# Kernel tuning notes

Hardware: AMD Instinct MI355X
Metric: run time of the kernel (lower is better)

The kernel has to match this reference:

```python
import jax, jax.numpy as jnp
import numpy as np

MAX_WARPING_WINDOW = None  # matches init kwarg (None => full window, no masking)


def _pairwise_euclidean(x, y):
    # x: (B, F, Tx), y: (B, F, Ty) -> (B, Tx, Ty)
    # ||x_t - y_s||_2 computed via the expanded quadratic form (one GEMM instead
    # of materializing the (B, F, Tx, Ty) difference tensor like the torch code).
    x2 = jnp.sum(x * x, axis=1)                      # (B, Tx)
    y2 = jnp.sum(y * y, axis=1)                      # (B, Ty)
    xy = jnp.einsum('bft,bfs->bts', x, y)            # (B, Tx, Ty)
    d2 = jnp.maximum(x2[:, :, None] + y2[:, None, :] - 2.0 * xy, 0.0)
    return jnp.sqrt(d2)


def _dtw(cost):
    # cost: (B, Tx, Ty). Classic DTW DP:
    #   dtw[i, j] = cost[i-1, j-1] + min(dtw[i-1, j], dtw[i, j-1], dtw[i-1, j-1])
    # outer scan over rows i, inner scan over columns j (carries dtw[i, j-1]).
    B, Tx, Ty = cost.shape
    dt = cost.dtype
    INF = jnp.array(jnp.inf, dt)
    cost_t = jnp.transpose(cost, (1, 2, 0))          # (Tx, Ty, B)

    def row_step(carry, cost_row):
        prev_row, left = carry                       # prev_row: (Ty, B) = dtw[i-1, 1:], left: (B,) = dtw[i-1, 0]
        prev_shift = jnp.concatenate([left[None, :], prev_row[:-1]], axis=0)  # dtw[i-1, j-1]
        a = jnp.minimum(prev_row, prev_shift)        # min(dtw[i-1, j], dtw[i-1, j-1])

        def col_step(cur_left, ac):
            a_j, c_j = ac                            # each (B,)
            cur = c_j + jnp.minimum(a_j, cur_left)   # cur_left = dtw[i, j-1]
            return cur, cur

        _, cur_row = jax.lax.scan(col_step, jnp.full((B,), INF, dt), (a, cost_row))
        return (cur_row, jnp.full((B,), INF, dt)), None

    # row 0 of the DP: dtw[0, 0] = 0, dtw[0, j>0] = inf
    init = (jnp.full((Ty, B), INF, dt), jnp.zeros((B,), dt))
    (last_row, _), _ = jax.lax.scan(row_step, init, cost_t)
    return last_row[-1]                              # dtw[Tx, Ty], shape (B,)


def setup_inputs() -> dict:
    key = jax.random.key(0)
    kx, ky = jax.random.split(key)
    B, F, T = 128, 128, 512
    x = jax.random.normal(kx, (B, F, T), dtype=jnp.float32)
    y = jax.random.normal(ky, (B, F, T), dtype=jnp.float32)
    return {"x": x, "y": y}


def reference(x, y):
    cost = _pairwise_euclidean(x, y)                 # (B, Tx, Ty)
    if MAX_WARPING_WINDOW is not None:
        Tx, Ty = cost.shape[1], cost.shape[2]
        p = jnp.arange(Tx)[:, None]
        q = jnp.arange(Ty)[None, :]
        cost = jnp.where(jnp.abs(p - q) <= MAX_WARPING_WINDOW, cost, jnp.inf)
    return _dtw(cost)
```

## Files before the change

kernel.cpp:

```cpp
#include <hip/hip_runtime.h>
#include <stdint.h>

#define B_ 128
#define F_ 128
#define T_ 512
#define TS 64
#define DIAG_N 1024

#define BIGV 1e30f

typedef __attribute__((ext_vector_type(8))) short     bf16x8;
typedef __attribute__((ext_vector_type(4))) float     f32x4;

static __device__ __forceinline__ unsigned short f32_to_bf16(float f) {
    union { float f; uint32_t u; } v; v.f = f;
    const uint32_t u = v.u + 0x7fffu + ((v.u >> 16) & 1u);
    return (unsigned short)(u >> 16);
}

static __device__ __forceinline__ float wave_shr1(float src, float fill) {
    const int r = __builtin_amdgcn_update_dpp(
        __builtin_bit_cast(int, fill), __builtin_bit_cast(int, src),
        0x138 , 0xf, 0xf, false);
    return __builtin_bit_cast(float, r);
}
static __device__ __forceinline__ float wave_shl1(float src, float fill) {
    const int r = __builtin_amdgcn_update_dpp(
        __builtin_bit_cast(int, fill), __builtin_bit_cast(int, src),
        0x130 , 0xf, 0xf, false);
    return __builtin_bit_cast(float, r);
}

#define FMIX_LO(dst, h, m)                                                  \
    asm("v_fma_mix_f32 %0, %1, 1.0, %2 op_sel:[0,0,0] op_sel_hi:[1,0,0]"    \
        : "=v"(dst) : "v"(h), "v"(m))
#define FMIX_HI(dst, h, m)                                                  \
    asm("v_fma_mix_f32 %0, %1, 1.0, %2 op_sel:[1,0,0] op_sel_hi:[1,0,0]"    \
        : "=v"(dst) : "v"(h), "v"(m))

__global__ __launch_bounds__(256) void dtw_prep_kernel(
    const float* __restrict__ x, const float* __restrict__ y,
    unsigned short* __restrict__ xt, unsigned short* __restrict__ yt,
    float* __restrict__ nx, float* __restrict__ ny)
{
    const int tch = blockIdx.x;
    const int b   = blockIdx.y;
    const int z   = blockIdx.z;
    const int tid = threadIdx.x;
    const int t0  = tch * 64;

    const float* src      = (z == 0 ? x : y) + (size_t)b * F_ * T_;
    unsigned short* dst   = (z == 0 ? xt : yt) + (size_t)b * T_ * F_;
    float* nd             = (z == 0 ? nx : ny) + (size_t)b * T_;

    __shared__ float S[F_][65];

    const int fr = tid >> 4;
    const int q  = (tid & 15) * 4;
#pragma unroll
    for (int p = 0; p < 8; ++p) {
        const int f = p * 16 + fr;
        const float4 v = *(const float4*)(src + (size_t)f * T_ + t0 + q);
        S[f][q] = v.x; S[f][q + 1] = v.y; S[f][q + 2] = v.z; S[f][q + 3] = v.w;
    }
    __syncthreads();

    if (tid < 64) {
        float s = 0.f;
#pragma unroll
        for (int f = 0; f < F_; ++f) { const float v = S[f][tid]; s = fmaf(v, v, s); }
        nd[t0 + tid] = s;
    }

    const int tl = tid >> 2;
    const int fb = (tid & 3) * 32;
    uint32_t pk[16];
#pragma unroll
    for (int e = 0; e < 16; ++e) {
        const uint32_t lo = f32_to_bf16(S[fb + 2 * e][tl]);
        const uint32_t hi = f32_to_bf16(S[fb + 2 * e + 1][tl]);
        pk[e] = lo | (hi << 16);
    }
    uint32_t* o = (uint32_t*)(dst + (size_t)(t0 + tl) * F_ + fb);
#pragma unroll
    for (int e = 0; e < 16; e += 4)
        *(uint4*)(o + e) = make_uint4(pk[e], pk[e + 1], pk[e + 2], pk[e + 3]);
}

__global__ __launch_bounds__(256) void dtw_cost_kernel(
    const unsigned short* __restrict__ xt, const unsigned short* __restrict__ yt,
    const float* __restrict__ nx, const float* __restrict__ ny,
    unsigned short* __restrict__ costD, int b0)
{
    const int tj  = blockIdx.x;
    const int ti  = blockIdx.y;
    const int bl  = blockIdx.z;
    const int b   = b0 + bl;
    const int tid = threadIdx.x;
    const int gi0 = ti * TS;
    const int gj0 = tj * TS;

    const int w    = tid >> 6;
    const int lane = tid & 63;
    const int l15  = lane & 15;
    const int hi   = lane >> 4;

    __shared__ __align__(16) char smem[16384];
    unsigned short* Ys = (unsigned short*)smem;

    {
        const int l16 = tid & 15;
#pragma unroll
        for (int p = 0; p < 4; ++p) {
            const int row = p * 16 + (tid >> 4);
            const uint4 vy = *(const uint4*)(yt + ((size_t)b * T_ + gj0 + row) * F_ + l16 * 8);
            const int byt = (row * 256 + l16 * 16) ^ ((row & 7) << 4);
            *(uint4*)((char*)Ys + byt) = vy;
        }
    }

    const unsigned short* xb = xt + ((size_t)b * T_ + gi0 + 16 * w + l15) * F_ + hi * 8;
    const bf16x8 A0 = *(const bf16x8*)(xb);
    const bf16x8 A1 = *(const bf16x8*)(xb + 32);
    const bf16x8 A2 = *(const bf16x8*)(xb + 64);
    const bf16x8 A3 = *(const bf16x8*)(xb + 96);

    const float4 x2r = *(const float4*)(nx + (size_t)b * T_ + gi0 + 16 * w + 4 * hi);
    float y2c[4];
#pragma unroll
    for (int nt = 0; nt < 4; ++nt)
        y2c[nt] = ny[(size_t)b * T_ + gj0 + nt * 16 + l15];
    const float x2v[4] = {x2r.x, x2r.y, x2r.z, x2r.w};

    __syncthreads();

    f32x4 acc[4] = {};
#pragma unroll
    for (int kb = 0; kb < 4; ++kb) {
        const int koff = kb * 64 + hi * 16;
        const bf16x8 a = (kb == 0) ? A0 : (kb == 1) ? A1 : (kb == 2) ? A2 : A3;
#pragma unroll
        for (int nt = 0; nt < 4; ++nt) {
            const int col = nt * 16 + l15;
            const bf16x8 bb = *(const bf16x8*)((const char*)Ys +
                               ((col * 256 + koff) ^ ((col & 7) << 4)));
            acc[nt] = __builtin_amdgcn_mfma_f32_16x16x32_bf16(a, bb, acc[nt], 0, 0, 0);
        }
    }

    __syncthreads();
    unsigned short* Ts = (unsigned short*)smem;
#pragma unroll
    for (int nt = 0; nt < 4; ++nt) {
        const int col = nt * 16 + l15;
#pragma unroll
        for (int r = 0; r < 4; ++r) {
            const int row = 16 * w + hi * 4 + r;
            const float c = sqrtf(fmaxf(x2v[r] + y2c[nt] - 2.f * acc[nt][r], 0.f));
            const _Float16 hv = (_Float16)c;
            Ts[row * 67 + col] = *(const unsigned short*)&hv;
        }
    }
    __syncthreads();

    unsigned short* outD = costD + (size_t)bl * (DIAG_N * (size_t)T_);
    const int tbase = gi0 + gj0;
#pragma unroll
    for (int q = 0; q < 16; ++q) {
        const int g = q * 4 + w;
        const int d = (lane <= g) ? g : g + 64;
        outD[(size_t)(tbase + d) * T_ + gj0 + lane] = Ts[(d - lane) * 67 + lane];
    }
}

__global__ __launch_bounds__(128, 1) void dtw_dp_bidi(
    const unsigned short* __restrict__ costD, float* __restrict__ out, int b0)
{
    const int bl  = blockIdx.x;
    const int tid = threadIdx.x;
    const int w   = tid >> 6;
    const int L   = tid & 63;
    const unsigned short* gbase = costD + (size_t)bl * (DIAG_N * (size_t)T_) + 8 * L;

    __shared__ __align__(16) unsigned short ringF[32][T_];
    __shared__ __align__(16) unsigned short ringB[32][T_];
    __shared__ __align__(16) float bb2[T_];
    __shared__ __align__(16) float bb3[T_];

    float va0 = BIGV, va1 = BIGV, va2 = BIGV, va3 = BIGV,
          va4 = BIGV, va5 = BIGV, va6 = BIGV, va7 = BIGV;
    float vb0 = BIGV, vb1 = BIGV, vb2 = BIGV, vb3 = BIGV,
          vb4 = BIGV, vb5 = BIGV, vb6 = BIGV, vb7 = BIGV;
    float s2c;
    uint4 ca0, ca1, ca2, ca3, ca4, ca5, ca6, ca7;
    uint4 cb0, cb1, cb2, cb3, cb4, cb5, cb6, cb7;

#define GLD(RING, row, slot)                                                \
    __builtin_amdgcn_global_load_lds(                                       \
        (const __attribute__((address_space(1))) void*)(gbase + (size_t)(row) * T_), \
        (__attribute__((address_space(3))) void*)(&RING[slot][0]), 16, 0, 0)

#define GLD8F(blk) do {                                                     \
    const int r0_ = (blk) * 8, s0_ = ((blk) & 3) * 8;                       \
    GLD(ringF, r0_ + 0, s0_ + 0); GLD(ringF, r0_ + 1, s0_ + 1);             \
    GLD(ringF, r0_ + 2, s0_ + 2); GLD(ringF, r0_ + 3, s0_ + 3);             \
    GLD(ringF, r0_ + 4, s0_ + 4); GLD(ringF, r0_ + 5, s0_ + 5);             \
    GLD(ringF, r0_ + 6, s0_ + 6); GLD(ringF, r0_ + 7, s0_ + 7);             \
} while (0)

#define GLD8B(blk) do {                                                     \
    const int v0_ = (blk) * 8, s0_ = ((blk) & 3) * 8;                       \
    GLD(ringB, 1022 - (v0_ + 0), s0_ + 0); GLD(ringB, 1022 - (v0_ + 1), s0_ + 1); \
    GLD(ringB, 1022 - (v0_ + 2), s0_ + 2); GLD(ringB, 1022 - (v0_ + 3), s0_ + 3); \
    GLD(ringB, 1022 - (v0_ + 4), s0_ + 4); GLD(ringB, 1022 - (v0_ + 5), s0_ + 5); \
    GLD(ringB, 1022 - (v0_ + 6), s0_ + 6); GLD(ringB, 1022 - (v0_ + 7), s0_ + 7); \
} while (0)

#define WAITV(n)                                                            \
    do { asm volatile("s_waitcnt vmcnt(" #n ")" ::: "memory");              \
         __builtin_amdgcn_sched_barrier(0); } while (0)

#define SB __builtin_amdgcn_sched_barrier(0)

#define RL8(RING, BK, blk) do {                                             \
    const unsigned short* rp_ = &RING[((blk) & 3) * 8][8 * L];              \
    BK##0 = *(const uint4*)(rp_ + 0 * T_);                                  \
    BK##1 = *(const uint4*)(rp_ + 1 * T_);                                  \
    BK##2 = *(const uint4*)(rp_ + 2 * T_);                                  \
    BK##3 = *(const uint4*)(rp_ + 3 * T_);                                  \
    BK##4 = *(const uint4*)(rp_ + 4 * T_);                                  \
    BK##5 = *(const uint4*)(rp_ + 5 * T_);                                  \
    BK##6 = *(const uint4*)(rp_ + 6 * T_);                                  \
    BK##7 = *(const uint4*)(rp_ + 7 * T_);                                  \
} while (0)

#define STEPF_A(Hv) do {                                                    \
    const float s1 = wave_shr1(va7, BIGV);                                  \
    float n0, n1, n2, n3, n4, n5, n6, n7;                                   \
    FMIX_LO(n0, Hv.x, fminf(fminf(va0, s1),  s2c));                         \
    FMIX_HI(n1, Hv.x, fminf(fminf(va1, va0), vb0));                         \
    FMIX_LO(n2, Hv.y, fminf(fminf(va2, va1), vb1));                         \
    FMIX_HI(n3, Hv.y, fminf(fminf(va3, va2), vb2));                         \
    FMIX_LO(n4, Hv.z, fminf(fminf(va4, va3), vb3));                         \
    FMIX_HI(n5, Hv.z, fminf(fminf(va5, va4), vb4));                         \
    FMIX_LO(n6, Hv.w, fminf(fminf(va6, va5), vb5));                         \
    FMIX_HI(n7, Hv.w, fminf(fminf(va7, va6), vb6));                         \
    s2c = s1;                                                               \
    vb0 = n0; vb1 = n1; vb2 = n2; vb3 = n3;                                 \
    vb4 = n4; vb5 = n5; vb6 = n6; vb7 = n7;                                 \
} while (0)

#define STEPF_B(Hv) do {                                                    \
    const float s1 = wave_shr1(vb7, BIGV);                                  \
    float n0, n1, n2, n3, n4, n5, n6, n7;                                   \
    FMIX_LO(n0, Hv.x, fminf(fminf(vb0, s1),  s2c));                         \
    FMIX_HI(n1, Hv.x, fminf(fminf(vb1, vb0), va0));                         \
    FMIX_LO(n2, Hv.y, fminf(fminf(vb2, vb1), va1));                         \
    FMIX_HI(n3, Hv.y, fminf(fminf(vb3, vb2), va2));                         \
    FMIX_LO(n4, Hv.z, fminf(fminf(vb4, vb3), va3));                         \
    FMIX_HI(n5, Hv.z, fminf(fminf(vb5, vb4), va4));                         \
    FMIX_LO(n6, Hv.w, fminf(fminf(vb6, vb5), va5));                         \
    FMIX_HI(n7, Hv.w, fminf(fminf(vb7, vb6), va6));                         \
    s2c = s1;                                                               \
    va0 = n0; va1 = n1; va2 = n2; va3 = n3;                                 \
    va4 = n4; va5 = n5; va6 = n6; va7 = n7;                                 \
} while (0)

#define STEPB_A(Hv) do {                                                    \
    const float s1 = wave_shl1(va0, BIGV);                                  \
    float n0, n1, n2, n3, n4, n5, n6, n7;                                   \
    FMIX_HI(n7, Hv.w, fminf(fminf(va7, s1),  s2c));                         \
    FMIX_LO(n6, Hv.w, fminf(fminf(va6, va7), vb7));                         \
    FMIX_HI(n5, Hv.z, fminf(fminf(va5, va6), vb6));                         \
    FMIX_LO(n4, Hv.z, fminf(fminf(va4, va5), vb5));                         \
    FMIX_HI(n3, Hv.y, fminf(fminf(va3, va4), vb4));                         \
    FMIX_LO(n2, Hv.y, fminf(fminf(va2, va3), vb3));                         \
    FMIX_HI(n1, Hv.x, fminf(fminf(va1, va2), vb2));                         \
    FMIX_LO(n0, Hv.x, fminf(fminf(va0, va1), vb1));                         \
    s2c = s1;                                                               \
    vb0 = n0; vb1 = n1; vb2 = n2; vb3 = n3;                                 \
    vb4 = n4; vb5 = n5; vb6 = n6; vb7 = n7;                                 \
} while (0)

#define STEPB_B(Hv) do {                                                    \
    const float s1 = wave_shl1(vb0, BIGV);                                  \
    float n0, n1, n2, n3, n4, n5, n6, n7;                                   \
    FMIX_HI(n7, Hv.w, fminf(fminf(vb7, s1),  s2c));                         \
    FMIX_LO(n6, Hv.w, fminf(fminf(vb6, vb7), va7));                         \
    FMIX_HI(n5, Hv.z, fminf(fminf(vb5, vb6), va6));                         \
    FMIX_LO(n4, Hv.z, fminf(fminf(vb4, vb5), va5));                         \
    FMIX_HI(n3, Hv.y, fminf(fminf(vb3, vb4), va4));                         \
    FMIX_LO(n2, Hv.y, fminf(fminf(vb2, vb3), va3));                         \
    FMIX_HI(n1, Hv.x, fminf(fminf(vb1, vb2), va2));                         \
    FMIX_LO(n0, Hv.x, fminf(fminf(vb0, vb1), va1));                         \
    s2c = s1;                                                               \
    va0 = n0; va1 = n1; va2 = n2; va3 = n3;                                 \
    va4 = n4; va5 = n5; va6 = n6; va7 = n7;                                 \
} while (0)

#define STEPF8(BK)                                                          \
    STEPF_A(BK##0); STEPF_B(BK##1); STEPF_A(BK##2); STEPF_B(BK##3);         \
    STEPF_A(BK##4); STEPF_B(BK##5); STEPF_A(BK##6); STEPF_B(BK##7)
#define STEPB8(BK)                                                          \
    STEPB_A(BK##0); STEPB_B(BK##1); STEPB_A(BK##2); STEPB_B(BK##3);         \
    STEPB_A(BK##4); STEPB_B(BK##5); STEPB_A(BK##6); STEPB_B(BK##7)

    if (w == 0) {
        s2c = (L == 0) ? 0.f : BIGV;
#pragma unroll
        for (int r = 0; r < 32; ++r) GLD(ringF, r, r);
        WAITV(24); RL8(ringF, ca, 0); SB;
        int k = 0;
#pragma unroll 1
        for (int it = 0; it < 30; ++it) {
            WAITV(16); RL8(ringF, cb, k + 1); SB; STEPF8(ca); SB; GLD8F(k + 4); SB;
            WAITV(16); RL8(ringF, ca, k + 2); SB; STEPF8(cb); SB; GLD8F(k + 5); SB;
            k += 2;
        }
        WAITV(16); RL8(ringF, cb, 61); SB; STEPF8(ca); SB;
        WAITV(8);  RL8(ringF, ca, 62); SB; STEPF8(cb); SB;
        WAITV(0);  RL8(ringF, cb, 63); SB; STEPF8(ca); SB;
        STEPF8(cb);
    } else {
        s2c = (L == 63) ? 0.f : BIGV;
#pragma unroll
        for (int r = 0; r < 32; ++r) GLD(ringB, 1022 - r, r);
        WAITV(24); RL8(ringB, ca, 0); SB;
        int k = 0;
#pragma unroll 1
        for (int it = 0; it < 30; ++it) {
            WAITV(16); RL8(ringB, cb, k + 1); SB; STEPB8(ca); SB; GLD8B(k + 4); SB;
            WAITV(16); RL8(ringB, ca, k + 2); SB; STEPB8(cb); SB; GLD8B(k + 5); SB;
            k += 2;
        }
        WAITV(16); RL8(ringB, cb, 61); SB; STEPB8(ca); SB;
        WAITV(8);  RL8(ringB, ca, 62); SB; STEPB8(cb); SB;
        WAITV(0);  RL8(ringB, cb, 63); SB; STEPB8(ca); SB;
        STEPB_A(cb0); STEPB_B(cb1); STEPB_A(cb2); STEPB_B(cb3);
        STEPB_A(cb4); STEPB_B(cb5); STEPB_A(cb6);
        *(float4*)&bb2[8 * L]     = make_float4(vb0, vb1, vb2, vb3);
        *(float4*)&bb2[8 * L + 4] = make_float4(vb4, vb5, vb6, vb7);
        *(float4*)&bb3[8 * L]     = make_float4(va0, va1, va2, va3);
        *(float4*)&bb3[8 * L + 4] = make_float4(va4, va5, va6, va7);
    }

    __syncthreads();

    if (w == 0) {
        const float4 p0 = *(const float4*)&bb2[8 * L];
        const float4 p1 = *(const float4*)&bb2[8 * L + 4];
        const float4 q0 = *(const float4*)&bb3[8 * L];
        const float4 q1 = *(const float4*)&bb3[8 * L + 4];
        const float b2[8] = {p0.x, p0.y, p0.z, p0.w, p1.x, p1.y, p1.z, p1.w};
        const float b3[8] = {q0.x, q0.y, q0.z, q0.w, q1.x, q1.y, q1.z, q1.w};
        const float F511[8] = {va0, va1, va2, va3, va4, va5, va6, va7};
        const float F510[8] = {vb0, vb1, vb2, vb3, vb4, vb5, vb6, vb7};
        float b2s[8], b3s[8];
#pragma unroll
        for (int kk = 0; kk < 7; ++kk) { b2s[kk] = b2[kk + 1]; b3s[kk] = b3[kk + 1]; }
        b2s[7] = wave_shl1(b2[0], BIGV);
        b3s[7] = wave_shl1(b3[0], BIGV);
        float m = BIGV;
#pragma unroll
        for (int kk = 0; kk < 8; ++kk) {
            const float t1 = F511[kk] + fminf(fminf(b2[kk], b2s[kk]), b3s[kk]);
            const float t2 = F510[kk] + b2s[kk];
            m = fminf(m, fminf(t1, t2));
        }
#pragma unroll
        for (int off = 1; off < 64; off <<= 1)
            m = fminf(m, __shfl_xor(m, off));
        if (L == 0) out[b0 + bl] = m;
    }

#undef GLD
#undef GLD8F
#undef GLD8B
#undef WAITV
#undef SB
#undef RL8
#undef STEPF_A
#undef STEPF_B
#undef STEPB_A
#undef STEPB_B
#undef STEPF8
#undef STEPB8
}

extern "C" void kernel_launch(void* const* d_in, const int* in_sizes, int n_in,
                              void* d_out, int out_size, void* d_ws, size_t ws_size,
                              hipStream_t stream)
{
    const float* x = (const float*)d_in[0];
    const float* y = (const float*)d_in[1];
    float* out = (float*)d_out;

    unsigned short* xt = (unsigned short*)d_ws;
    unsigned short* yt = xt + (size_t)B_ * T_ * F_;
    float* nx = (float*)(yt + (size_t)B_ * T_ * F_);
    float* ny = nx + (size_t)B_ * T_;
    unsigned short* costD = (unsigned short*)(ny + (size_t)B_ * T_);
    const size_t head = (size_t)((char*)costD - (char*)d_ws);

    const size_t perb = (size_t)DIAG_N * T_ * sizeof(unsigned short);
    int Bg = 8;
    for (int g = 128; g >= 8; g >>= 1)
        if (ws_size >= head + perb * (size_t)g) { Bg = g; break; }

    hipLaunchKernelGGL(dtw_prep_kernel, dim3(T_ / 64, B_, 2), dim3(256), 0, stream,
                       x, y, xt, yt, nx, ny);

    for (int b0 = 0; b0 < B_; b0 += Bg) {
        dim3 gc(T_ / TS, T_ / TS, Bg);
        hipLaunchKernelGGL(dtw_cost_kernel, gc, dim3(256), 0, stream,
                           xt, yt, nx, ny, costD, b0);
        hipLaunchKernelGGL(dtw_dp_bidi, dim3(Bg), dim3(128), 0, stream,
                           costD, out, b0);
    }
}
```

Baseline: 99.10 us.

## Split bidirectional DTW DP into separate per-direction workgroups with global combine

The forward and backward DP waves, previously two waves in one 128-thread block, now run as separate 64-thread blocks (2*Bg blocks) so they can be placed on different CUs. The half-results go to a global scratch buffer and a new small combine kernel finishes the reduction. Each block gets a deeper 64-row LDS ring with eight blocks of loads in flight to hide global latency better. The cost is an extra kernel launch per batch group, a global round-trip for the boundary rows, and a slightly larger workspace per batch, which may reduce the chosen Bg.

New measurement: 105.9 us. 1.07x slower.

```diff
diff --git a/kernel.cpp b/kernel.cpp
--- a/kernel.cpp
+++ b/kernel.cpp
@@ -21,13 +21,13 @@
 static __device__ __forceinline__ float wave_shr1(float src, float fill) {
     const int r = __builtin_amdgcn_update_dpp(
         __builtin_bit_cast(int, fill), __builtin_bit_cast(int, src),
-        0x138 , 0xf, 0xf, false);
+        0x138, 0xf, 0xf, false);
     return __builtin_bit_cast(float, r);
 }
 static __device__ __forceinline__ float wave_shl1(float src, float fill) {
     const int r = __builtin_amdgcn_update_dpp(
         __builtin_bit_cast(int, fill), __builtin_bit_cast(int, src),
-        0x130 , 0xf, 0xf, false);
+        0x130, 0xf, 0xf, false);
     return __builtin_bit_cast(float, r);
 }
 
@@ -173,19 +173,15 @@
     }
 }
 
-__global__ __launch_bounds__(128, 1) void dtw_dp_bidi(
-    const unsigned short* __restrict__ costD, float* __restrict__ out, int b0)
+__global__ __launch_bounds__(64, 1) void dtw_dp_dir(
+    const unsigned short* __restrict__ costD, float* __restrict__ hand, int Bg)
 {
-    const int bl  = blockIdx.x;
-    const int tid = threadIdx.x;
-    const int w   = tid >> 6;
-    const int L   = tid & 63;
+    const int isB = (int)blockIdx.x >= Bg;
+    const int bl  = isB ? (int)blockIdx.x - Bg : (int)blockIdx.x;
+    const int L   = threadIdx.x;
     const unsigned short* gbase = costD + (size_t)bl * (DIAG_N * (size_t)T_) + 8 * L;
 
-    __shared__ __align__(16) unsigned short ringF[32][T_];
-    __shared__ __align__(16) unsigned short ringB[32][T_];
-    __shared__ __align__(16) float bb2[T_];
-    __shared__ __align__(16) float bb3[T_];
+    __shared__ __align__(16) unsigned short ring[64][T_];
 
     float va0 = BIGV, va1 = BIGV, va2 = BIGV, va3 = BIGV,
           va4 = BIGV, va5 = BIGV, va6 = BIGV, va7 = BIGV;
@@ -195,25 +191,25 @@
     uint4 ca0, ca1, ca2, ca3, ca4, ca5, ca6, ca7;
     uint4 cb0, cb1, cb2, cb3, cb4, cb5, cb6, cb7;
 
-#define GLD(RING, row, slot)                                                \
+#define GLD(row, slotrow)                                                   \
     __builtin_amdgcn_global_load_lds(                                       \
         (const __attribute__((address_space(1))) void*)(gbase + (size_t)(row) * T_), \
-        (__attribute__((address_space(3))) void*)(&RING[slot][0]), 16, 0, 0)
+        (__attribute__((address_space(3))) void*)(&ring[slotrow][0]), 16, 0, 0)
 
 #define GLD8F(blk) do {                                                     \
-    const int r0_ = (blk) * 8, s0_ = ((blk) & 3) * 8;                       \
-    GLD(ringF, r0_ + 0, s0_ + 0); GLD(ringF, r0_ + 1, s0_ + 1);             \
-    GLD(ringF, r0_ + 2, s0_ + 2); GLD(ringF, r0_ + 3, s0_ + 3);             \
-    GLD(ringF, r0_ + 4, s0_ + 4); GLD(ringF, r0_ + 5, s0_ + 5);             \
-    GLD(ringF, r0_ + 6, s0_ + 6); GLD(ringF, r0_ + 7, s0_ + 7);             \
+    const int r0_ = (blk) * 8, s0_ = ((blk) & 7) * 8;                       \
+    GLD(r0_ + 0, s0_ + 0); GLD(r0_ + 1, s0_ + 1);                           \
+    GLD(r0_ + 2, s0_ + 2); GLD(r0_ + 3, s0_ + 3);                           \
+    GLD(r0_ + 4, s0_ + 4); GLD(r0_ + 5, s0_ + 5);                           \
+    GLD(r0_ + 6, s0_ + 6); GLD(r0_ + 7, s0_ + 7);                           \
 } while (0)
 
 #define GLD8B(blk) do {                                                     \
-    const int v0_ = (blk) * 8, s0_ = ((blk) & 3) * 8;                       \
-    GLD(ringB, 1022 - (v0_ + 0), s0_ + 0); GLD(ringB, 1022 - (v0_ + 1), s0_ + 1); \
-    GLD(ringB, 1022 - (v0_ + 2), s0_ + 2); GLD(ringB, 1022 - (v0_ + 3), s0_ + 3); \
-    GLD(ringB, 1022 - (v0_ + 4), s0_ + 4); GLD(ringB, 1022 - (v0_ + 5), s0_ + 5); \
-    GLD(ringB, 1022 - (v0_ + 6), s0_ + 6); GLD(ringB, 1022 - (v0_ + 7), s0_ + 7); \
+    const int v0_ = (blk) * 8, s0_ = ((blk) & 7) * 8;                       \
+    GLD(1022 - (v0_ + 0), s0_ + 0); GLD(1022 - (v0_ + 1), s0_ + 1);         \
+    GLD(1022 - (v0_ + 2), s0_ + 2); GLD(1022 - (v0_ + 3), s0_ + 3);         \
+    GLD(1022 - (v0_ + 4), s0_ + 4); GLD(1022 - (v0_ + 5), s0_ + 5);         \
+    GLD(1022 - (v0_ + 6), s0_ + 6); GLD(1022 - (v0_ + 7), s0_ + 7);         \
 } while (0)
 
 #define WAITV(n)                                                            \
@@ -222,8 +218,8 @@
 
 #define SB __builtin_amdgcn_sched_barrier(0)
 
-#define RL8(RING, BK, blk) do {                                             \
-    const unsigned short* rp_ = &RING[((blk) & 3) * 8][8 * L];              \
+#define RL8(BK, blk) do {                                                   \
+    const unsigned short* rp_ = &ring[((blk) & 7) * 8][8 * L];              \
     BK##0 = *(const uint4*)(rp_ + 0 * T_);                                  \
     BK##1 = *(const uint4*)(rp_ + 1 * T_);                                  \
     BK##2 = *(const uint4*)(rp_ + 2 * T_);                                  \
@@ -305,72 +301,59 @@
     STEPB_A(BK##0); STEPB_B(BK##1); STEPB_A(BK##2); STEPB_B(BK##3);         \
     STEPB_A(BK##4); STEPB_B(BK##5); STEPB_A(BK##6); STEPB_B(BK##7)
 
-    if (w == 0) {
+    float* hb = hand + (size_t)bl * 4 * T_;
+
+    if (!isB) {
         s2c = (L == 0) ? 0.f : BIGV;
-#pragma unroll
-        for (int r = 0; r < 32; ++r) GLD(ringF, r, r);
-        WAITV(24); RL8(ringF, ca, 0); SB;
+        GLD8F(0); GLD8F(1); GLD8F(2); GLD8F(3);
+        GLD8F(4); GLD8F(5); GLD8F(6);
+        WAITV(48); RL8(ca, 0); SB;
+        GLD8F(7); SB;
         int k = 0;
 #pragma unroll 1
-        for (int it = 0; it < 30; ++it) {
-            WAITV(16); RL8(ringF, cb, k + 1); SB; STEPF8(ca); SB; GLD8F(k + 4); SB;
-            WAITV(16); RL8(ringF, ca, k + 2); SB; STEPF8(cb); SB; GLD8F(k + 5); SB;
+        for (int it = 0; it < 28; ++it) {
+            WAITV(48); RL8(cb, k + 1); SB; STEPF8(ca); SB; GLD8F(k + 8); SB;
+            WAITV(48); RL8(ca, k + 2); SB; STEPF8(cb); SB; GLD8F(k + 9); SB;
             k += 2;
         }
-        WAITV(16); RL8(ringF, cb, 61); SB; STEPF8(ca); SB;
-        WAITV(8);  RL8(ringF, ca, 62); SB; STEPF8(cb); SB;
-        WAITV(0);  RL8(ringF, cb, 63); SB; STEPF8(ca); SB;
+        WAITV(48); RL8(cb, 57); SB; STEPF8(ca); SB;
+        WAITV(40); RL8(ca, 58); SB; STEPF8(cb); SB;
+        WAITV(32); RL8(cb, 59); SB; STEPF8(ca); SB;
+        WAITV(24); RL8(ca, 60); SB; STEPF8(cb); SB;
+        WAITV(16); RL8(cb, 61); SB; STEPF8(ca); SB;
+        WAITV(8);  RL8(ca, 62); SB; STEPF8(cb); SB;
+        WAITV(0);  RL8(cb, 63); SB; STEPF8(ca); SB;
         STEPF8(cb);
+        *(float4*)(hb + 0 * T_ + 8 * L)     = make_float4(va0, va1, va2, va3);
+        *(float4*)(hb + 0 * T_ + 8 * L + 4) = make_float4(va4, va5, va6, va7);
+        *(float4*)(hb + 1 * T_ + 8 * L)     = make_float4(vb0, vb1, vb2, vb3);
+        *(float4*)(hb + 1 * T_ + 8 * L + 4) = make_float4(vb4, vb5, vb6, vb7);
     } else {
         s2c = (L == 63) ? 0.f : BIGV;
-#pragma unroll
-        for (int r = 0; r < 32; ++r) GLD(ringB, 1022 - r, r);
-        WAITV(24); RL8(ringB, ca, 0); SB;
+        GLD8B(0); GLD8B(1); GLD8B(2); GLD8B(3);
+        GLD8B(4); GLD8B(5); GLD8B(6);
+        WAITV(48); RL8(ca, 0); SB;
+        GLD8B(7); SB;
         int k = 0;
 #pragma unroll 1
-        for (int it = 0; it < 30; ++it) {
-            WAITV(16); RL8(ringB, cb, k + 1); SB; STEPB8(ca); SB; GLD8B(k + 4); SB;
-            WAITV(16); RL8(ringB, ca, k + 2); SB; STEPB8(cb); SB; GLD8B(k + 5); SB;
+        for (int it = 0; it < 28; ++it) {
+            WAITV(48); RL8(cb, k + 1); SB; STEPB8(ca); SB; GLD8B(k + 8); SB;
+            WAITV(48); RL8(ca, k + 2); SB; STEPB8(cb); SB; GLD8B(k + 9); SB;
             k += 2;
         }
-        WAITV(16); RL8(ringB, cb, 61); SB; STEPB8(ca); SB;
-        WAITV(8);  RL8(ringB, ca, 62); SB; STEPB8(cb); SB;
-        WAITV(0);  RL8(ringB, cb, 63); SB; STEPB8(ca); SB;
+        WAITV(48); RL8(cb, 57); SB; STEPB8(ca); SB;
+        WAITV(40); RL8(ca, 58); SB; STEPB8(cb); SB;
+        WAITV(32); RL8(cb, 59); SB; STEPB8(ca); SB;
+        WAITV(24); RL8(ca, 60); SB; STEPB8(cb); SB;
+        WAITV(16); RL8(cb, 61); SB; STEPB8(ca); SB;
+        WAITV(8);  RL8(ca, 62); SB; STEPB8(cb); SB;
+        WAITV(0);  RL8(cb, 63); SB; STEPB8(ca); SB;
         STEPB_A(cb0); STEPB_B(cb1); STEPB_A(cb2); STEPB_B(cb3);
         STEPB_A(cb4); STEPB_B(cb5); STEPB_A(cb6);
-        *(float4*)&bb2[8 * L]     = make_float4(vb0, vb1, vb2, vb3);
-        *(float4*)&bb2[8 * L + 4] = make_float4(vb4, vb5, vb6, vb7);
-        *(float4*)&bb3[8 * L]     = make_float4(va0, va1, va2, va3);
-        *(float4*)&bb3[8 * L + 4] = make_float4(va4, va5, va6, va7);
-    }
-
-    __syncthreads();
-
-    if (w == 0) {
-        const float4 p0 = *(const float4*)&bb2[8 * L];
-        const float4 p1 = *(const float4*)&bb2[8 * L + 4];
-        const float4 q0 = *(const float4*)&bb3[8 * L];
-        const float4 q1 = *(const float4*)&bb3[8 * L + 4];
-        const float b2[8] = {p0.x, p0.y, p0.z, p0.w, p1.x, p1.y, p1.z, p1.w};
-        const float b3[8] = {q0.x, q0.y, q0.z, q0.w, q1.x, q1.y, q1.z, q1.w};
-        const float F511[8] = {va0, va1, va2, va3, va4, va5, va6, va7};
-        const float F510[8] = {vb0, vb1, vb2, vb3, vb4, vb5, vb6, vb7};
-        float b2s[8], b3s[8];
-#pragma unroll
-        for (int kk = 0; kk < 7; ++kk) { b2s[kk] = b2[kk + 1]; b3s[kk] = b3[kk + 1]; }
-        b2s[7] = wave_shl1(b2[0], BIGV);
-        b3s[7] = wave_shl1(b3[0], BIGV);
-        float m = BIGV;
-#pragma unroll
-        for (int kk = 0; kk < 8; ++kk) {
-            const float t1 = F511[kk] + fminf(fminf(b2[kk], b2s[kk]), b3s[kk]);
-            const float t2 = F510[kk] + b2s[kk];
-            m = fminf(m, fminf(t1, t2));
-        }
-#pragma unroll
-        for (int off = 1; off < 64; off <<= 1)
-            m = fminf(m, __shfl_xor(m, off));
-        if (L == 0) out[b0 + bl] = m;
+        *(float4*)(hb + 2 * T_ + 8 * L)     = make_float4(vb0, vb1, vb2, vb3);
+        *(float4*)(hb + 2 * T_ + 8 * L + 4) = make_float4(vb4, vb5, vb6, vb7);
+        *(float4*)(hb + 3 * T_ + 8 * L)     = make_float4(va0, va1, va2, va3);
+        *(float4*)(hb + 3 * T_ + 8 * L + 4) = make_float4(va4, va5, va6, va7);
     }
 
 #undef GLD
@@ -387,6 +370,46 @@
 #undef STEPB8
 }
 
+__global__ __launch_bounds__(64) void dtw_combine(
+    const float* __restrict__ hand, float* __restrict__ out, int b0)
+{
+    const int bl = blockIdx.x;
+    const int L  = threadIdx.x;
+    const float* hb = hand + (size_t)bl * 4 * T_;
+
+    const float4 f0 = *(const float4*)(hb + 0 * T_ + 8 * L);
+    const float4 f1 = *(const float4*)(hb + 0 * T_ + 8 * L + 4);
+    const float4 g0 = *(const float4*)(hb + 1 * T_ + 8 * L);
+    const float4 g1 = *(const float4*)(hb + 1 * T_ + 8 * L + 4);
+    const float4 p0 = *(const float4*)(hb + 2 * T_ + 8 * L);
+    const float4 p1 = *(const float4*)(hb + 2 * T_ + 8 * L + 4);
+    const float4 q0 = *(const float4*)(hb + 3 * T_ + 8 * L);
+    const float4 q1 = *(const float4*)(hb + 3 * T_ + 8 * L + 4);
+
+    const float F511[8] = {f0.x, f0.y, f0.z, f0.w, f1.x, f1.y, f1.z, f1.w};
+    const float F510[8] = {g0.x, g0.y, g0.z, g0.w, g1.x, g1.y, g1.z, g1.w};
+    const float b2[8]   = {p0.x, p0.y, p0.z, p0.w, p1.x, p1.y, p1.z, p1.w};
+    const float b3[8]   = {q0.x, q0.y, q0.z, q0.w, q1.x, q1.y, q1.z, q1.w};
+
+    float b2s[8], b3s[8];
+#pragma unroll
+    for (int kk = 0; kk < 7; ++kk) { b2s[kk] = b2[kk + 1]; b3s[kk] = b3[kk + 1]; }
+    b2s[7] = wave_shl1(b2[0], BIGV);
+    b3s[7] = wave_shl1(b3[0], BIGV);
+
+    float m = BIGV;
+#pragma unroll
+    for (int kk = 0; kk < 8; ++kk) {
+        const float t1 = F511[kk] + fminf(fminf(b2[kk], b2s[kk]), b3s[kk]);
+        const float t2 = F510[kk] + b2s[kk];
+        m = fminf(m, fminf(t1, t2));
+    }
+#pragma unroll
+    for (int off = 1; off < 64; off <<= 1)
+        m = fminf(m, __shfl_xor(m, off));
+    if (L == 0) out[b0 + bl] = m;
+}
+
 extern "C" void kernel_launch(void* const* d_in, const int* in_sizes, int n_in,
                               void* d_out, int out_size, void* d_ws, size_t ws_size,
                               hipStream_t stream)
@@ -402,10 +425,13 @@
     unsigned short* costD = (unsigned short*)(ny + (size_t)B_ * T_);
     const size_t head = (size_t)((char*)costD - (char*)d_ws);
 
-    const size_t perb = (size_t)DIAG_N * T_ * sizeof(unsigned short);
+    const size_t perb = (size_t)DIAG_N * T_ * sizeof(unsigned short)
+                      + (size_t)4 * T_ * sizeof(float);
     int Bg = 8;
     for (int g = 128; g >= 8; g >>= 1)
         if (ws_size >= head + perb * (size_t)g) { Bg = g; break; }
+
+    float* hand = (float*)(costD + (size_t)Bg * DIAG_N * T_);
 
     hipLaunchKernelGGL(dtw_prep_kernel, dim3(T_ / 64, B_, 2), dim3(256), 0, stream,
                        x, y, xt, yt, nx, ny);
@@ -414,7 +440,9 @@
         dim3 gc(T_ / TS, T_ / TS, Bg);
         hipLaunchKernelGGL(dtw_cost_kernel, gc, dim3(256), 0, stream,
                            xt, yt, nx, ny, costD, b0);
-        hipLaunchKernelGGL(dtw_dp_bidi, dim3(Bg), dim3(128), 0, stream,
-                           costD, out, b0);
-    }
-}
+        hipLaunchKernelGGL(dtw_dp_dir, dim3(2 * Bg), dim3(64), 0, stream,
+                           costD, hand, Bg);
+        hipLaunchKernelGGL(dtw_combine, dim3(Bg), dim3(64), 0, stream,
+                           hand, out, b0);
+    }
+}
```
